# Performance work log

Measured on AMD Instinct MI355X. Metric: run time of the kernel, lower is better.

## Reference

```python
import jax, jax.numpy as jnp
import numpy as np
import math

B, S, D, H, E = 4, 4096, 256, 8, 262144
HD = D // H
ITER_NUM = 4
TEMP = 1.0
LN_EPS = 1e-12
N = B * S


def setup_inputs() -> dict:
    key = jax.random.key(0)
    ks = jax.random.split(key, 6)
    return {
        "hidden_states": jax.random.normal(ks[0], (B, S, D), dtype=jnp.float32),
        "attention_mask": jnp.zeros((B, S), dtype=jnp.float32),
        "src": jax.random.randint(ks[1], (E,), 0, N),
        "dst": jax.random.randint(ks[2], (E,), 0, N),
        "Wqkv": jax.random.normal(ks[3], (D, 3 * D), dtype=jnp.float32) * 0.02,
        "bqkv": jnp.zeros((3 * D,), dtype=jnp.float32),
        "Wo": jax.random.normal(ks[4], (D, D), dtype=jnp.float32) * 0.02,
        "bo": jnp.zeros((D,), dtype=jnp.float32),
        "gamma": jnp.ones((D,), dtype=jnp.float32),
        "beta": jnp.zeros((D,), dtype=jnp.float32),
    }


def _gn_attn(hidden_states, attention_mask, src, dst, Wqkv, bqkv, Wo, bo, gamma, beta):
    # qkv projection (node ordering is batch-major: node = b*S + s)
    qkv = hidden_states @ Wqkv + bqkv                      # [B,S,3D]
    q, k, v = jnp.split(qkv, 3, axis=-1)
    q = q / math.sqrt(HD)
    qn = q.reshape(N, H, HD)
    kn = k.reshape(N, H, HD)
    vn = v.reshape(N, H, HD)
    node_mask = (attention_mask >= 0).reshape(N)           # [N] bool

    # per-edge dot-product scores: u_dot_v('k','q') -> dot(k[src], q[dst])
    score = jnp.einsum("ehd,ehd->eh", kn[src], qn[dst])    # [E,H]
    edge_mask = node_mask[src] & node_mask[dst]
    score = jnp.where(edge_mask[:, None], score, jnp.float32(-10000.0))

    # edge softmax over incoming edges of each dst node (per head)
    mx = jax.ops.segment_max(score, dst, num_segments=N)   # [N,H]
    es = jnp.exp(score - mx[dst])
    den = jax.ops.segment_sum(es, dst, num_segments=N)     # [N,H]
    attn = es / den[dst]                                   # [E,H]

    # diffusion (heat-kernel / PPR-style) message passing
    h = math.exp(-TEMP) * vn                               # [N,H,HD]
    gather = h
    fact = 1.0
    for ki in range(1, ITER_NUM):
        msg = attn[:, :, None] * h[src]                    # [E,H,HD]
        h = jax.ops.segment_sum(msg, dst, num_segments=N)  # [N,H,HD]
        fact = fact * (TEMP / ki)
        gather = gather + fact * h

    attn_out = gather.reshape(B, S, D)

    # output projection + residual + LayerNorm
    y = attn_out @ Wo + bo + hidden_states
    mu = jnp.mean(y, axis=-1, keepdims=True)
    var = jnp.mean(jnp.square(y - mu), axis=-1, keepdims=True)
    return (y - mu) / jnp.sqrt(var + LN_EPS) * gamma + beta


def reference(hidden_states, attention_mask, src, dst, Wqkv, bqkv, Wo, bo, gamma, beta):
    return _gn_attn(hidden_states, attention_mask, src, dst, Wqkv, bqkv, Wo, bo, gamma, beta)
```

## Files before the change

kernel.cpp:

```cpp
#include <hip/hip_runtime.h>
#include <math.h>

#define NN 16384
#define DD 256
#define HH 8
#define EE 262144
#define D3 768
#define QSCALE 0.17677669529663687f
#define EXPN1 0.36787944117144233f
#define LN_EPS 1e-12f

typedef short bf16x8 __attribute__((ext_vector_type(8)));
typedef float f32x4 __attribute__((ext_vector_type(4)));
typedef float f32x2 __attribute__((ext_vector_type(2)));
typedef unsigned short u16;
typedef unsigned char u8;

__device__ __forceinline__ float bf_lo(unsigned u) { return __uint_as_float(u << 16); }
__device__ __forceinline__ float bf_hi(unsigned u) { return __uint_as_float(u & 0xffff0000u); }
__device__ __forceinline__ unsigned f2bf(float f) {
    unsigned b = __float_as_uint(f);
    return (b + 0x7fffu + ((b >> 16) & 1u)) >> 16;
}
__device__ __forceinline__ unsigned pack2bf(float lo, float hi) {
    return f2bf(lo) | (f2bf(hi) << 16);
}
__device__ __forceinline__ u8 f2fp8(float v) {
    return (u8)(__builtin_amdgcn_cvt_pk_fp8_f32(v, v, 0, false) & 0xff);
}

__global__ void prep_kernel(const float* __restrict__ hidden, unsigned* __restrict__ hidb,
                            const float* __restrict__ Wqkv, const float* __restrict__ bqkv,
                            u16* __restrict__ WtQ, float* __restrict__ biasq,
                            const float* __restrict__ Wo, const float* __restrict__ bo,
                            u16* __restrict__ WtO, float* __restrict__ biaso,
                            const int* __restrict__ dst, int* __restrict__ deg) {
    int b = blockIdx.x;
    if (b < 4096) {
        int gid = b * 256 + threadIdx.x;
        float4 v = *(const float4*)(hidden + (size_t)gid * 4);
        *(uint2*)(hidb + (size_t)gid * 2) = make_uint2(pack2bf(v.x, v.y), pack2bf(v.z, v.w));
    } else if (b < 4864) {
        int gid = (b - 4096) * 256 + threadIdx.x;
        int n = gid >> 8, k = gid & 255;
        float s = (n < DD) ? QSCALE : 1.0f;
        WtQ[(size_t)n * 256 + k] = (u16)f2bf(Wqkv[(size_t)k * D3 + n] * s);
        if (k == 0) biasq[n] = bqkv[n] * s;
    } else if (b < 5120) {
        int gid = (b - 4864) * 256 + threadIdx.x;
        int n = gid >> 8, k = gid & 255;
        WtO[(size_t)n * 256 + k] = (u16)f2bf(Wo[(size_t)k * DD + n]);
        if (k == 0) biaso[n] = bo[n];
    } else {
        int e = (b - 5120) * 256 + threadIdx.x;
        atomicAdd(&deg[dst[e]], 1);
    }
}

__global__ __launch_bounds__(256) void mfma_gemm1_kernel(
        const u16* __restrict__ Ab, const u16* __restrict__ Bt,
        const float* __restrict__ bias,
        u16* __restrict__ qb, u8* __restrict__ kb8,
        u8* __restrict__ h8, u16* __restrict__ gb) {
    __shared__ u16 As[128 * 40];
    __shared__ u16 Bs[128 * 40];
    const int tid = threadIdx.x;
    const int m0 = blockIdx.y * 128;
    const int n0 = blockIdx.x * 128;
    const int wave = tid >> 6, lane = tid & 63;
    const int wr = wave >> 1, wc = wave & 1;
    const int lm = lane & 15, quad = lane >> 4;

    f32x4 acc[4][4] = {};
    const int r0 = tid >> 2;
    const int c8 = (tid & 3) * 8;

    for (int k0 = 0; k0 < 256; k0 += 32) {
        #pragma unroll
        for (int s = 0; s < 2; ++s) {
            int r = r0 + s * 64;
            *(uint4*)&As[r * 40 + c8] = *(const uint4*)(Ab + (size_t)(m0 + r) * 256 + k0 + c8);
            *(uint4*)&Bs[r * 40 + c8] = *(const uint4*)(Bt + (size_t)(n0 + r) * 256 + k0 + c8);
        }
        __syncthreads();
        bf16x8 af[4], bfv[4];
        #pragma unroll
        for (int mi = 0; mi < 4; ++mi)
            af[mi] = *(const bf16x8*)&As[(wr * 64 + mi * 16 + lm) * 40 + quad * 8];
        #pragma unroll
        for (int ni = 0; ni < 4; ++ni)
            bfv[ni] = *(const bf16x8*)&Bs[(wc * 64 + ni * 16 + lm) * 40 + quad * 8];
        #pragma unroll
        for (int mi = 0; mi < 4; ++mi)
            #pragma unroll
            for (int ni = 0; ni < 4; ++ni)
                acc[mi][ni] = __builtin_amdgcn_mfma_f32_16x16x32_bf16(
                    af[mi], bfv[ni], acc[mi][ni], 0, 0, 0);
        __syncthreads();
    }

    const int type = n0 >> 8;
    const int cb = n0 & 255;
    #pragma unroll
    for (int mi = 0; mi < 4; ++mi) {
        #pragma unroll
        for (int j = 0; j < 4; ++j) {
            int m = m0 + wr * 64 + mi * 16 + quad * 4 + j;
            #pragma unroll
            for (int ni = 0; ni < 4; ++ni) {
                int nl = wc * 64 + ni * 16 + lm;
                float val = acc[mi][ni][j] + bias[n0 + nl];
                size_t off = (size_t)m * 256 + cb + nl;
                if (type == 0) qb[off] = (u16)f2bf(val);
                else if (type == 1) kb8[off] = f2fp8(val);
                else {
                    float hx = val * EXPN1;
                    h8[off] = f2fp8(hx);
                    gb[off] = (u16)f2bf(hx);
                }
            }
        }
    }
}

__global__ __launch_bounds__(1024) void scan_kernel(const int* __restrict__ deg,
                                                    int* __restrict__ offs,
                                                    int* __restrict__ cursor, int n) {
    __shared__ int part[1024];
    int t = threadIdx.x;
    int base = t * 16;
    int local[16];
    int s = 0;
    #pragma unroll
    for (int i = 0; i < 16; ++i) { local[i] = s; s += deg[base + i]; }
    part[t] = s;
    __syncthreads();
    for (int d = 1; d < 1024; d <<= 1) {
        int add = (t >= d) ? part[t - d] : 0;
        __syncthreads();
        part[t] += add;
        __syncthreads();
    }
    int excl = part[t] - s;
    #pragma unroll
    for (int i = 0; i < 16; ++i) {
        offs[base + i] = excl + local[i];
        cursor[base + i] = excl + local[i];
    }
    if (t == 1023) offs[n] = excl + s;
}

__global__ void scatter_kernel(const int* __restrict__ src, const int* __restrict__ dst,
                               int* __restrict__ cursor, int* __restrict__ srcs) {
    int e = blockIdx.x * 256 + threadIdx.x;
    int pos = atomicAdd(&cursor[dst[e]], 1);
    srcs[pos] = src[e];
}

__global__ __launch_bounds__(256) void edge_softmax_kernel(
        const unsigned* __restrict__ qb, const u8* __restrict__ kb8,
        const int* __restrict__ offs, const int* __restrict__ srcs,
        const float* __restrict__ amask, float* __restrict__ attn,
        float* __restrict__ inv) {
    const int wave = threadIdx.x >> 6, lane = threadIdx.x & 63;
    const int node = blockIdx.x * 4 + wave;
    const int h = lane & 7;
    const int eo = lane >> 3;
    const int beg = offs[node], end = offs[node + 1];
    const uint4* qp = (const uint4*)(qb + (size_t)node * 128 + h * 16);
    uint4 q0 = qp[0], q1 = qp[1], q2 = qp[2], q3 = qp[3];
    unsigned qq[16] = {q0.x, q0.y, q0.z, q0.w, q1.x, q1.y, q1.z, q1.w,
                       q2.x, q2.y, q2.z, q2.w, q3.x, q3.y, q3.z, q3.w};
    const bool dvalid = amask[node] >= 0.0f;

    float m = -1e30f;
    for (int i0 = beg; i0 < end; i0 += 8) {
        int i = i0 + eo;
        if (i < end) {
            int s = srcs[i];
            const uint4* kp = (const uint4*)(kb8 + (size_t)s * 256 + h * 32);
            uint4 k0 = kp[0], k1 = kp[1];
            unsigned kk[8] = {k0.x, k0.y, k0.z, k0.w, k1.x, k1.y, k1.z, k1.w};
            float acc = 0.0f;
            #pragma unroll
            for (int t = 0; t < 8; ++t) {
                f32x2 a = __builtin_amdgcn_cvt_pk_f32_fp8(kk[t], false);
                f32x2 b = __builtin_amdgcn_cvt_pk_f32_fp8(kk[t], true);
                acc += a.x * bf_lo(qq[2 * t]) + a.y * bf_hi(qq[2 * t]);
                acc += b.x * bf_lo(qq[2 * t + 1]) + b.y * bf_hi(qq[2 * t + 1]);
            }
            bool valid = dvalid && (amask[s] >= 0.0f);
            float score = valid ? acc : -10000.0f;
            attn[(size_t)i * 8 + h] = score;
            m = fmaxf(m, score);
        }
    }
    m = fmaxf(m, __shfl_xor(m, 8));
    m = fmaxf(m, __shfl_xor(m, 16));
    m = fmaxf(m, __shfl_xor(m, 32));

    float den = 0.0f;
    for (int i0 = beg; i0 < end; i0 += 8) {
        int i = i0 + eo;
        if (i < end) {
            float es = __expf(attn[(size_t)i * 8 + h] - m);
            attn[(size_t)i * 8 + h] = es;
            den += es;
        }
    }
    den += __shfl_xor(den, 8);
    den += __shfl_xor(den, 16);
    den += __shfl_xor(den, 32);
    if (lane < 8) inv[node * 8 + h] = (end > beg) ? 1.0f / den : 0.0f;
}

__global__ void diffuse_kernel(const int* __restrict__ offs, const int* __restrict__ srcs,
                               const float* __restrict__ attn, const float* __restrict__ inv,
                               const unsigned* __restrict__ hcur, unsigned* __restrict__ hnext,
                               uint2* __restrict__ gb, float fact) {
    int gid = blockIdx.x * 256 + threadIdx.x;
    int node = gid >> 6;
    int j2 = gid & 63;
    int h = j2 >> 3;
    int beg = offs[node], end = offs[node + 1];
    float a0 = 0.0f, a1 = 0.0f, a2 = 0.0f, a3 = 0.0f;
    int i = beg;
    for (; i + 8 <= end; i += 8) {
        int sarr[8]; float aarr[8]; unsigned hv[8];
        #pragma unroll
        for (int t = 0; t < 8; ++t) {
            sarr[t] = srcs[i + t];
            aarr[t] = attn[(size_t)(i + t) * 8 + h];
        }
        #pragma unroll
        for (int t = 0; t < 8; ++t) hv[t] = hcur[(size_t)sarr[t] * 64 + j2];
        #pragma unroll
        for (int t = 0; t < 8; ++t) {
            float a = aarr[t];
            f32x2 lo = __builtin_amdgcn_cvt_pk_f32_fp8(hv[t], false);
            f32x2 hi = __builtin_amdgcn_cvt_pk_f32_fp8(hv[t], true);
            a0 += a * lo.x; a1 += a * lo.y;
            a2 += a * hi.x; a3 += a * hi.y;
        }
    }
    if (i < end) {
        int cnt = end - i;
        int sarr[8]; float aarr[8]; unsigned hv[8];
        #pragma unroll
        for (int t = 0; t < 8; ++t) if (t < cnt) {
            sarr[t] = srcs[i + t];
            aarr[t] = attn[(size_t)(i + t) * 8 + h];
        }
        #pragma unroll
        for (int t = 0; t < 8; ++t) if (t < cnt) hv[t] = hcur[(size_t)sarr[t] * 64 + j2];
        #pragma unroll
        for (int t = 0; t < 8; ++t) if (t < cnt) {
            float a = aarr[t];
            f32x2 lo = __builtin_amdgcn_cvt_pk_f32_fp8(hv[t], false);
            f32x2 hi = __builtin_amdgcn_cvt_pk_f32_fp8(hv[t], true);
            a0 += a * lo.x; a1 += a * lo.y;
            a2 += a * hi.x; a3 += a * hi.y;
        }
    }
    float iv = inv[node * 8 + h];
    a0 *= iv; a1 *= iv; a2 *= iv; a3 *= iv;
    if (hnext) {
        int pk = __builtin_amdgcn_cvt_pk_fp8_f32(a0, a1, 0, false);
        pk = __builtin_amdgcn_cvt_pk_fp8_f32(a2, a3, pk, true);
        hnext[(size_t)node * 64 + j2] = (unsigned)pk;
    }
    uint2* gp = gb + (size_t)node * 64 + j2;
    uint2 g = *gp;
    float g0 = bf_lo(g.x) + fact * a0;
    float g1 = bf_hi(g.x) + fact * a1;
    float g2 = bf_lo(g.y) + fact * a2;
    float g3 = bf_hi(g.y) + fact * a3;
    *gp = make_uint2(pack2bf(g0, g1), pack2bf(g2, g3));
}

__global__ __launch_bounds__(256) void gemm2_ln_kernel(
        const u16* __restrict__ Ab, const u16* __restrict__ Bt,
        const float* __restrict__ bias, const float* __restrict__ resid,
        const float* __restrict__ gamma, const float* __restrict__ beta,
        float* __restrict__ out) {
    __shared__ u16 As[64 * 40];
    __shared__ u16 Bs[256 * 40];
    const int tid = threadIdx.x;
    const int m0 = blockIdx.x * 64;
    const int wave = tid >> 6, lane = tid & 63;
    const int lm = lane & 15, quad = lane >> 4;

    f32x4 acc[16] = {};
    for (int k0 = 0; k0 < 256; k0 += 32) {
        *(uint4*)&As[(tid >> 2) * 40 + (tid & 3) * 8] =
            *(const uint4*)(Ab + (size_t)(m0 + (tid >> 2)) * 256 + k0 + (tid & 3) * 8);
        {
            const uint4* srcp = (const uint4*)(Bt + (size_t)tid * 256 + k0);
            uint4* dstp = (uint4*)&Bs[tid * 40];
            dstp[0] = srcp[0]; dstp[1] = srcp[1]; dstp[2] = srcp[2]; dstp[3] = srcp[3];
        }
        __syncthreads();
        bf16x8 af = *(const bf16x8*)&As[(wave * 16 + lm) * 40 + quad * 8];
        #pragma unroll
        for (int ni = 0; ni < 16; ++ni) {
            bf16x8 bfv = *(const bf16x8*)&Bs[(ni * 16 + lm) * 40 + quad * 8];
            acc[ni] = __builtin_amdgcn_mfma_f32_16x16x32_bf16(af, bfv, acc[ni], 0, 0, 0);
        }
        __syncthreads();
    }

    const int mrow = m0 + wave * 16 + quad * 4;
    float ga[16], be[16];
    float rowsum[4] = {}, rowsq[4] = {};
    #pragma unroll
    for (int ni = 0; ni < 16; ++ni) {
        int col = ni * 16 + lm;
        float bia = bias[col];
        ga[ni] = gamma[col]; be[ni] = beta[col];
        #pragma unroll
        for (int j = 0; j < 4; ++j) {
            float val = acc[ni][j] + bia + resid[(size_t)(mrow + j) * 256 + col];
            acc[ni][j] = val;
            rowsum[j] += val;
            rowsq[j] += val * val;
        }
    }
    #pragma unroll
    for (int j = 0; j < 4; ++j) {
        #pragma unroll
        for (int msk = 1; msk <= 8; msk <<= 1) {
            rowsum[j] += __shfl_xor(rowsum[j], msk);
            rowsq[j] += __shfl_xor(rowsq[j], msk);
        }
    }
    float mu[4], rstd[4];
    #pragma unroll
    for (int j = 0; j < 4; ++j) {
        mu[j] = rowsum[j] * (1.0f / 256.0f);
        float var = rowsq[j] * (1.0f / 256.0f) - mu[j] * mu[j];
        rstd[j] = 1.0f / sqrtf(var + LN_EPS);
    }
    #pragma unroll
    for (int ni = 0; ni < 16; ++ni) {
        int col = ni * 16 + lm;
        #pragma unroll
        for (int j = 0; j < 4; ++j)
            out[(size_t)(mrow + j) * 256 + col] = (acc[ni][j] - mu[j]) * rstd[j] * ga[ni] + be[ni];
    }
}

extern "C" void kernel_launch(void* const* d_in, const int* in_sizes, int n_in,
                              void* d_out, int out_size, void* d_ws, size_t ws_size,
                              hipStream_t stream) {
    const float* hidden = (const float*)d_in[0];
    const float* amask  = (const float*)d_in[1];
    const int*   src    = (const int*)d_in[2];
    const int*   dst    = (const int*)d_in[3];
    const float* Wqkv   = (const float*)d_in[4];
    const float* bqkv   = (const float*)d_in[5];
    const float* Wo     = (const float*)d_in[6];
    const float* bo     = (const float*)d_in[7];
    const float* gamma  = (const float*)d_in[8];
    const float* beta   = (const float*)d_in[9];
    float* out = (float*)d_out;

    char* p = (char*)d_ws;
    u16*      hidb   = (u16*)p;      p += (size_t)NN * DD * 2;
    u16*      WtQ    = (u16*)p;      p += (size_t)D3 * DD * 2;
    u16*      WtO    = (u16*)p;      p += (size_t)DD * DD * 2;
    float*    biasq  = (float*)p;    p += (size_t)D3 * 4;
    float*    biaso  = (float*)p;    p += (size_t)DD * 4;
    u16*      qb     = (u16*)p;      p += (size_t)NN * DD * 2;
    u8*       kb8    = (u8*)p;       p += (size_t)NN * DD;
    u8*       h8A    = (u8*)p;       p += (size_t)NN * DD;
    u8*       h8B    = (u8*)p;       p += (size_t)NN * DD;
    u16*      gb     = (u16*)p;      p += (size_t)NN * DD * 2;
    float*    attn   = (float*)p;    p += (size_t)EE * HH * 4;
    float*    inv    = (float*)p;    p += (size_t)NN * HH * 4;
    int*      deg    = (int*)p;      p += (size_t)NN * 4;
    int*      offs   = (int*)p;      p += (size_t)(NN + 1) * 4;
    int*      cursor = (int*)p;      p += (size_t)NN * 4;
    int*      srcs   = (int*)p;      p += (size_t)EE * 4;

    hipMemsetAsync(deg, 0, (size_t)NN * 4, stream);
    prep_kernel<<<6144, 256, 0, stream>>>(hidden, (unsigned*)hidb,
                                          Wqkv, bqkv, WtQ, biasq,
                                          Wo, bo, WtO, biaso, dst, deg);

    scan_kernel<<<1, 1024, 0, stream>>>(deg, offs, cursor, NN);
    scatter_kernel<<<EE / 256, 256, 0, stream>>>(src, dst, cursor, srcs);

    mfma_gemm1_kernel<<<dim3(D3 / 128, NN / 128), 256, 0, stream>>>(
        hidb, WtQ, biasq, qb, kb8, h8A, gb);

    edge_softmax_kernel<<<NN / 4, 256, 0, stream>>>(
        (const unsigned*)qb, kb8, offs, srcs, amask, attn, inv);

    diffuse_kernel<<<(NN * 64) / 256, 256, 0, stream>>>(
        offs, srcs, attn, inv, (const unsigned*)h8A, (unsigned*)h8B, (uint2*)gb, 1.0f);
    diffuse_kernel<<<(NN * 64) / 256, 256, 0, stream>>>(
        offs, srcs, attn, inv, (const unsigned*)h8B, (unsigned*)h8A, (uint2*)gb, 0.5f);
    diffuse_kernel<<<(NN * 64) / 256, 256, 0, stream>>>(
        offs, srcs, attn, inv, (const unsigned*)h8A, nullptr, (uint2*)gb, 1.0f / 6.0f);

    gemm2_ln_kernel<<<NN / 64, 256, 0, stream>>>(
        gb, WtO, biaso, hidden, gamma, beta, out);
}
```

Before: 225.2 us.

## Fuse scatter into GEMM1, single-pass softmax without max, bf16 attention, nontemporal accesses

Merges the CSR scatter kernel into the QKV GEMM launch as extra blocks, so the two kernels become one launch and can overlap. The edge softmax drops the max-subtraction pass and computes exp directly, storing unnormalised weights as bf16, which halves attention-weight traffic and removes one read/write sweep. It also adds nontemporal loads and stores in several kernels and merges the diffuse loop's main and tail paths into one. Skipping the max shift risks overflow for large scores, and bf16 weights lose precision.

Result: slower. 292.0 us (+29.7%).

```diff
diff --git a/kernel.cpp b/kernel.cpp
--- a/kernel.cpp
+++ b/kernel.cpp
@@ -13,11 +13,14 @@
 typedef short bf16x8 __attribute__((ext_vector_type(8)));
 typedef float f32x4 __attribute__((ext_vector_type(4)));
 typedef float f32x2 __attribute__((ext_vector_type(2)));
+typedef unsigned u32x4 __attribute__((ext_vector_type(4)));
+typedef unsigned u32x2 __attribute__((ext_vector_type(2)));
 typedef unsigned short u16;
 typedef unsigned char u8;
 
 __device__ __forceinline__ float bf_lo(unsigned u) { return __uint_as_float(u << 16); }
 __device__ __forceinline__ float bf_hi(unsigned u) { return __uint_as_float(u & 0xffff0000u); }
+__device__ __forceinline__ float bf16u(u16 u) { return __uint_as_float(((unsigned)u) << 16); }
 __device__ __forceinline__ unsigned f2bf(float f) {
     unsigned b = __float_as_uint(f);
     return (b + 0x7fffu + ((b >> 16) & 1u)) >> 16;
@@ -57,16 +60,51 @@
     }
 }
 
-__global__ __launch_bounds__(256) void mfma_gemm1_kernel(
+__global__ __launch_bounds__(1024) void scan_kernel(const int* __restrict__ deg,
+                                                    int* __restrict__ offs,
+                                                    int* __restrict__ cursor, int n) {
+    __shared__ int part[1024];
+    int t = threadIdx.x;
+    int base = t * 16;
+    int local[16];
+    int s = 0;
+    #pragma unroll
+    for (int i = 0; i < 16; ++i) { local[i] = s; s += deg[base + i]; }
+    part[t] = s;
+    __syncthreads();
+    for (int d = 1; d < 1024; d <<= 1) {
+        int add = (t >= d) ? part[t - d] : 0;
+        __syncthreads();
+        part[t] += add;
+        __syncthreads();
+    }
+    int excl = part[t] - s;
+    #pragma unroll
+    for (int i = 0; i < 16; ++i) {
+        offs[base + i] = excl + local[i];
+        cursor[base + i] = excl + local[i];
+    }
+    if (t == 1023) offs[n] = excl + s;
+}
+
+__global__ __launch_bounds__(256) void gemm1_scatter_kernel(
         const u16* __restrict__ Ab, const u16* __restrict__ Bt,
         const float* __restrict__ bias,
         u16* __restrict__ qb, u8* __restrict__ kb8,
-        u8* __restrict__ h8, u16* __restrict__ gb) {
+        u8* __restrict__ h8, u16* __restrict__ gb,
+        const int* __restrict__ src, const int* __restrict__ dst,
+        int* __restrict__ cursor, int* __restrict__ srcs) {
     __shared__ u16 As[128 * 40];
     __shared__ u16 Bs[128 * 40];
     const int tid = threadIdx.x;
-    const int m0 = blockIdx.y * 128;
-    const int n0 = blockIdx.x * 128;
+    if (blockIdx.x >= 768) {
+        int e = (blockIdx.x - 768) * 256 + tid;
+        int pos = atomicAdd(&cursor[dst[e]], 1);
+        srcs[pos] = src[e];
+        return;
+    }
+    const int n0 = (blockIdx.x % 6) * 128;
+    const int m0 = (blockIdx.x / 6) * 128;
     const int wave = tid >> 6, lane = tid & 63;
     const int wr = wave >> 1, wc = wave & 1;
     const int lm = lane & 15, quad = lane >> 4;
@@ -123,57 +161,26 @@
     }
 }
 
-__global__ __launch_bounds__(1024) void scan_kernel(const int* __restrict__ deg,
-                                                    int* __restrict__ offs,
-                                                    int* __restrict__ cursor, int n) {
-    __shared__ int part[1024];
-    int t = threadIdx.x;
-    int base = t * 16;
-    int local[16];
-    int s = 0;
-    #pragma unroll
-    for (int i = 0; i < 16; ++i) { local[i] = s; s += deg[base + i]; }
-    part[t] = s;
-    __syncthreads();
-    for (int d = 1; d < 1024; d <<= 1) {
-        int add = (t >= d) ? part[t - d] : 0;
-        __syncthreads();
-        part[t] += add;
-        __syncthreads();
-    }
-    int excl = part[t] - s;
-    #pragma unroll
-    for (int i = 0; i < 16; ++i) {
-        offs[base + i] = excl + local[i];
-        cursor[base + i] = excl + local[i];
-    }
-    if (t == 1023) offs[n] = excl + s;
-}
-
-__global__ void scatter_kernel(const int* __restrict__ src, const int* __restrict__ dst,
-                               int* __restrict__ cursor, int* __restrict__ srcs) {
-    int e = blockIdx.x * 256 + threadIdx.x;
-    int pos = atomicAdd(&cursor[dst[e]], 1);
-    srcs[pos] = src[e];
-}
-
 __global__ __launch_bounds__(256) void edge_softmax_kernel(
         const unsigned* __restrict__ qb, const u8* __restrict__ kb8,
         const int* __restrict__ offs, const int* __restrict__ srcs,
-        const float* __restrict__ amask, float* __restrict__ attn,
+        const float* __restrict__ amask, u16* __restrict__ attn16,
         float* __restrict__ inv) {
     const int wave = threadIdx.x >> 6, lane = threadIdx.x & 63;
     const int node = blockIdx.x * 4 + wave;
     const int h = lane & 7;
     const int eo = lane >> 3;
     const int beg = offs[node], end = offs[node + 1];
-    const uint4* qp = (const uint4*)(qb + (size_t)node * 128 + h * 16);
-    uint4 q0 = qp[0], q1 = qp[1], q2 = qp[2], q3 = qp[3];
+    const u32x4* qp = (const u32x4*)(qb + (size_t)node * 128 + h * 16);
+    u32x4 q0 = __builtin_nontemporal_load(qp);
+    u32x4 q1 = __builtin_nontemporal_load(qp + 1);
+    u32x4 q2 = __builtin_nontemporal_load(qp + 2);
+    u32x4 q3 = __builtin_nontemporal_load(qp + 3);
     unsigned qq[16] = {q0.x, q0.y, q0.z, q0.w, q1.x, q1.y, q1.z, q1.w,
                        q2.x, q2.y, q2.z, q2.w, q3.x, q3.y, q3.z, q3.w};
     const bool dvalid = amask[node] >= 0.0f;
 
-    float m = -1e30f;
+    float den = 0.0f;
     for (int i0 = beg; i0 < end; i0 += 8) {
         int i = i0 + eo;
         if (i < end) {
@@ -190,66 +197,35 @@
                 acc += b.x * bf_lo(qq[2 * t + 1]) + b.y * bf_hi(qq[2 * t + 1]);
             }
             bool valid = dvalid && (amask[s] >= 0.0f);
-            float score = valid ? acc : -10000.0f;
-            attn[(size_t)i * 8 + h] = score;
-            m = fmaxf(m, score);
-        }
-    }
-    m = fmaxf(m, __shfl_xor(m, 8));
-    m = fmaxf(m, __shfl_xor(m, 16));
-    m = fmaxf(m, __shfl_xor(m, 32));
-
-    float den = 0.0f;
-    for (int i0 = beg; i0 < end; i0 += 8) {
-        int i = i0 + eo;
-        if (i < end) {
-            float es = __expf(attn[(size_t)i * 8 + h] - m);
-            attn[(size_t)i * 8 + h] = es;
+            float es = valid ? __expf(acc) : 0.0f;
+            __builtin_nontemporal_store((u16)f2bf(es), &attn16[(size_t)i * 8 + h]);
             den += es;
         }
     }
     den += __shfl_xor(den, 8);
     den += __shfl_xor(den, 16);
     den += __shfl_xor(den, 32);
-    if (lane < 8) inv[node * 8 + h] = (end > beg) ? 1.0f / den : 0.0f;
-}
-
-__global__ void diffuse_kernel(const int* __restrict__ offs, const int* __restrict__ srcs,
-                               const float* __restrict__ attn, const float* __restrict__ inv,
-                               const unsigned* __restrict__ hcur, unsigned* __restrict__ hnext,
-                               uint2* __restrict__ gb, float fact) {
+    if (lane < 8) inv[node * 8 + lane] = (den > 0.0f) ? 1.0f / den : 0.0f;
+}
+
+__global__ __launch_bounds__(256) void diffuse_kernel(
+        const int* __restrict__ offs, const int* __restrict__ srcs,
+        const u16* __restrict__ attn16, const float* __restrict__ inv,
+        const unsigned* __restrict__ hcur, unsigned* __restrict__ hnext,
+        u32x2* __restrict__ gb, float fact) {
     int gid = blockIdx.x * 256 + threadIdx.x;
     int node = gid >> 6;
     int j2 = gid & 63;
     int h = j2 >> 3;
     int beg = offs[node], end = offs[node + 1];
     float a0 = 0.0f, a1 = 0.0f, a2 = 0.0f, a3 = 0.0f;
-    int i = beg;
-    for (; i + 8 <= end; i += 8) {
+    for (int i0 = beg; i0 < end; i0 += 8) {
+        int cnt = end - i0; if (cnt > 8) cnt = 8;
         int sarr[8]; float aarr[8]; unsigned hv[8];
         #pragma unroll
-        for (int t = 0; t < 8; ++t) {
-            sarr[t] = srcs[i + t];
-            aarr[t] = attn[(size_t)(i + t) * 8 + h];
-        }
-        #pragma unroll
-        for (int t = 0; t < 8; ++t) hv[t] = hcur[(size_t)sarr[t] * 64 + j2];
-        #pragma unroll
-        for (int t = 0; t < 8; ++t) {
-            float a = aarr[t];
-            f32x2 lo = __builtin_amdgcn_cvt_pk_f32_fp8(hv[t], false);
-            f32x2 hi = __builtin_amdgcn_cvt_pk_f32_fp8(hv[t], true);
-            a0 += a * lo.x; a1 += a * lo.y;
-            a2 += a * hi.x; a3 += a * hi.y;
-        }
-    }
-    if (i < end) {
-        int cnt = end - i;
-        int sarr[8]; float aarr[8]; unsigned hv[8];
-        #pragma unroll
         for (int t = 0; t < 8; ++t) if (t < cnt) {
-            sarr[t] = srcs[i + t];
-            aarr[t] = attn[(size_t)(i + t) * 8 + h];
+            sarr[t] = srcs[i0 + t];
+            aarr[t] = bf16u(__builtin_nontemporal_load(&attn16[(size_t)(i0 + t) * 8 + h]));
         }
         #pragma unroll
         for (int t = 0; t < 8; ++t) if (t < cnt) hv[t] = hcur[(size_t)sarr[t] * 64 + j2];
@@ -269,13 +245,13 @@
         pk = __builtin_amdgcn_cvt_pk_fp8_f32(a2, a3, pk, true);
         hnext[(size_t)node * 64 + j2] = (unsigned)pk;
     }
-    uint2* gp = gb + (size_t)node * 64 + j2;
-    uint2 g = *gp;
-    float g0 = bf_lo(g.x) + fact * a0;
-    float g1 = bf_hi(g.x) + fact * a1;
-    float g2 = bf_lo(g.y) + fact * a2;
-    float g3 = bf_hi(g.y) + fact * a3;
-    *gp = make_uint2(pack2bf(g0, g1), pack2bf(g2, g3));
+    u32x2* gp = gb + (size_t)node * 64 + j2;
+    u32x2 g = __builtin_nontemporal_load(gp);
+    u32x2 ng;
+    ng.x = pack2bf(bf_lo(g.x) + fact * a0, bf_hi(g.x) + fact * a1);
+    ng.y = pack2bf(bf_lo(g.y) + fact * a2, bf_hi(g.y) + fact * a3);
+    if (hnext) __builtin_nontemporal_store(ng, gp);
+    else *gp = ng;
 }
 
 __global__ __launch_bounds__(256) void gemm2_ln_kernel(
@@ -319,7 +295,8 @@
         ga[ni] = gamma[col]; be[ni] = beta[col];
         #pragma unroll
         for (int j = 0; j < 4; ++j) {
-            float val = acc[ni][j] + bia + resid[(size_t)(mrow + j) * 256 + col];
+            float val = acc[ni][j] + bia +
+                        __builtin_nontemporal_load(&resid[(size_t)(mrow + j) * 256 + col]);
             acc[ni][j] = val;
             rowsum[j] += val;
             rowsq[j] += val * val;
@@ -345,7 +322,9 @@
         int col = ni * 16 + lm;
         #pragma unroll
         for (int j = 0; j < 4; ++j)
-            out[(size_t)(mrow + j) * 256 + col] = (acc[ni][j] - mu[j]) * rstd[j] * ga[ni] + be[ni];
+            __builtin_nontemporal_store(
+                (acc[ni][j] - mu[j]) * rstd[j] * ga[ni] + be[ni],
+                &out[(size_t)(mrow + j) * 256 + col]);
     }
 }
 
@@ -375,7 +354,7 @@
     u8*       h8A    = (u8*)p;       p += (size_t)NN * DD;
     u8*       h8B    = (u8*)p;       p += (size_t)NN * DD;
     u16*      gb     = (u16*)p;      p += (size_t)NN * DD * 2;
-    float*    attn   = (float*)p;    p += (size_t)EE * HH * 4;
+    u16*      attn16 = (u16*)p;      p += (size_t)EE * HH * 2;
     float*    inv    = (float*)p;    p += (size_t)NN * HH * 4;
     int*      deg    = (int*)p;      p += (size_t)NN * 4;
     int*      offs   = (int*)p;      p += (size_t)(NN + 1) * 4;
@@ -388,20 +367,19 @@
                                           Wo, bo, WtO, biaso, dst, deg);
 
     scan_kernel<<<1, 1024, 0, stream>>>(deg, offs, cursor, NN);
-    scatter_kernel<<<EE / 256, 256, 0, stream>>>(src, dst, cursor, srcs);
-
-    mfma_gemm1_kernel<<<dim3(D3 / 128, NN / 128), 256, 0, stream>>>(
-        hidb, WtQ, biasq, qb, kb8, h8A, gb);
+
+    gemm1_scatter_kernel<<<1792, 256, 0, stream>>>(
+        hidb, WtQ, biasq, qb, kb8, h8A, gb, src, dst, cursor, srcs);
 
     edge_softmax_kernel<<<NN / 4, 256, 0, stream>>>(
-        (const unsigned*)qb, kb8, offs, srcs, amask, attn, inv);
+        (const unsigned*)qb, kb8, offs, srcs, amask, attn16, inv);
 
     diffuse_kernel<<<(NN * 64) / 256, 256, 0, stream>>>(
-        offs, srcs, attn, inv, (const unsigned*)h8A, (unsigned*)h8B, (uint2*)gb, 1.0f);
+        offs, srcs, attn16, inv, (const unsigned*)h8A, (unsigned*)h8B, (u32x2*)gb, 1.0f);
     diffuse_kernel<<<(NN * 64) / 256, 256, 0, stream>>>(
-        offs, srcs, attn, inv, (const unsigned*)h8B, (unsigned*)h8A, (uint2*)gb, 0.5f);
+        offs, srcs, attn16, inv, (const unsigned*)h8B, (unsigned*)h8A, (u32x2*)gb, 0.5f);
     diffuse_kernel<<<(NN * 64) / 256, 256, 0, stream>>>(
-        offs, srcs, attn, inv, (const unsigned*)h8A, nullptr, (uint2*)gb, 1.0f / 6.0f);
+        offs, srcs, attn16, inv, (const unsigned*)h8A, nullptr, (u32x2*)gb, 1.0f / 6.0f);
 
     gemm2_ln_kernel<<<NN / 64, 256, 0, stream>>>(
         gb, WtO, biaso, hidden, gamma, beta, out);
```
